# Performance work log

Hardware: AMD Instinct MI355X
Metric: run time of the kernel (lower is better)

## Reference

```python
import jax, jax.numpy as jnp
import numpy as np

EMBED_DIM = 2048
NUM_HEADS = 16
HEAD_DIM = EMBED_DIM // NUM_HEADS
EPS = 1e-6


def setup_inputs() -> dict:
    key = jax.random.key(0)
    ks = jax.random.split(key, 12)
    B, S, D = 4, 2048, EMBED_DIM
    s = 1.0 / np.sqrt(D)
    return {
        "query": jax.random.normal(ks[0], (B, S, D), jnp.float32),
        "key": jax.random.normal(ks[1], (B, S, D), jnp.float32),
        "value": jax.random.normal(ks[2], (B, S, D), jnp.float32),
        "Wq": jax.random.normal(ks[3], (D, D), jnp.float32) * s,
        "bq": jnp.zeros((D,), jnp.float32),
        "Wk": jax.random.normal(ks[4], (D, D), jnp.float32) * s,
        "bk": jnp.zeros((D,), jnp.float32),
        "Wv": jax.random.normal(ks[5], (D, D), jnp.float32) * s,
        "bv": jnp.zeros((D,), jnp.float32),
        "Wo": jax.random.normal(ks[6], (D, D), jnp.float32) * s,
        "bo": jnp.zeros((D,), jnp.float32),
        "q_norm_w": jnp.ones((HEAD_DIM,), jnp.float32),
        "k_norm_w": jnp.ones((HEAD_DIM,), jnp.float32),
    }


def _rms_norm(x, w):
    # RMSNorm over last dim (head_dim): x / sqrt(mean(x^2)+eps) * w
    ms = jnp.mean(jnp.square(x), axis=-1, keepdims=True)
    return x * jax.lax.rsqrt(ms + EPS) * w


def reference(query, key, value, Wq, bq, Wk, bk, Wv, bv, Wo, bo, q_norm_w, k_norm_w):
    B, Nq, D = query.shape
    Nk = key.shape[1]
    H, Hd = NUM_HEADS, HEAD_DIM
    # torch nn.Linear: y = x @ W.T + b
    q = (query @ Wq.T + bq).reshape(B, Nq, H, Hd).transpose(0, 2, 1, 3)  # (B,H,Nq,Hd)
    k = (key @ Wk.T + bk).reshape(B, Nk, H, Hd).transpose(0, 2, 1, 3)
    v = (value @ Wv.T + bv).reshape(B, Nk, H, Hd).transpose(0, 2, 1, 3)
    q = _rms_norm(q, q_norm_w)
    k = _rms_norm(k, k_norm_w)
    scale = 1.0 / np.sqrt(Hd)
    scores = jnp.einsum("bhqd,bhkd->bhqk", q, k) * scale  # (B,H,Nq,Nk)
    attn = jax.nn.softmax(scores, axis=-1)
    out = jnp.einsum("bhqk,bhkd->bhqd", attn, v)  # (B,H,Nq,Hd)
    out = out.transpose(0, 2, 1, 3).reshape(B, Nq, D)
    return out @ Wo.T + bo
```

## Files before the change

kernel.cpp:

```cpp
#include <hip/hip_runtime.h>

#define NB 4
#define NS 2048
#define ND 2048
#define NH 16
#define NHD 128

typedef __bf16 bf16;
typedef __attribute__((ext_vector_type(8))) __bf16 bf16x8;
typedef __attribute__((ext_vector_type(4))) __bf16 bf16x4;
typedef __attribute__((ext_vector_type(4))) float f32x4;
typedef __attribute__((ext_vector_type(16))) float f32x16;

#define MFMA(a, b, c) __builtin_amdgcn_mfma_f32_16x16x32_bf16(a, b, c, 0, 0, 0)
#define MFMA32(a, b, c) __builtin_amdgcn_mfma_f32_32x32x16_bf16(a, b, c, 0, 0, 0)

__device__ __forceinline__ void gload16(const bf16* g, bf16* l) {
    __builtin_amdgcn_global_load_lds(
        (const __attribute__((address_space(1))) void*)g,
        (__attribute__((address_space(3))) void*)l, 16, 0, 0);
}

#define BAR() do { asm volatile("" ::: "memory"); __builtin_amdgcn_s_barrier(); \
                   asm volatile("" ::: "memory"); } while (0)
#define VMCNT4() asm volatile("s_waitcnt vmcnt(4)" ::: "memory")
#define VMCNT0() asm volatile("s_waitcnt vmcnt(0)" ::: "memory")

enum { RA00 = 0, RA01 = 16384, RA10 = 32768, RA11 = 49152,
       RB00 = 65536, RB01 = 81920, RB10 = 98304, RB11 = 114688 };

__device__ __forceinline__ void stage_half(const bf16* gcorner, char* lds_region,
                                           int w, int lane, int scol) {
    const bf16* g = gcorner + (size_t)(w * 16 + (lane >> 3)) * ND + scol;
    gload16(g, (bf16*)(lds_region + w * 2048));
    gload16(g + (size_t)8 * ND, (bf16*)(lds_region + w * 2048 + 1024));
}

__device__ __forceinline__ void lds_loadA(const char* pool, int region, int mi0,
                                          int l15, int quad, bf16x8 (&af)[8]) {
    const int flip = (l15 & 4) << 3;
    #pragma unroll
    for (int mi = 0; mi < 4; ++mi) {
        const int rb = region + ((mi0 + mi) * 16 + l15) * 128;
        #pragma unroll
        for (int kk = 0; kk < 2; ++kk)
            af[mi * 2 + kk] = *reinterpret_cast<const bf16x8*>(
                pool + rb + ((kk * 64 + quad * 16) ^ flip));
    }
}

template <int NI0>
__device__ __forceinline__ void lds_loadB(const char* pool, int region, int wn1,
                                          int l15, int quad, bf16x8 (&bfr)[8]) {
    const int flip = (l15 & 4) << 3;
    #pragma unroll
    for (int ni = 0; ni < 2; ++ni) {
        const int rb = region + (wn1 * 64 + (NI0 + ni) * 16 + l15) * 128;
        #pragma unroll
        for (int kk = 0; kk < 2; ++kk)
            bfr[(NI0 + ni) * 2 + kk] = *reinterpret_cast<const bf16x8*>(
                pool + rb + ((kk * 64 + quad * 16) ^ flip));
    }
}

template <int MI0, int NI0>
__device__ __forceinline__ void mfma_quad(f32x4 (&acc)[8][4], const bf16x8 (&af)[8],
                                          const bf16x8 (&bfr)[8]) {
    __builtin_amdgcn_s_setprio(1);
    #pragma unroll
    for (int mi = 0; mi < 4; ++mi)
        #pragma unroll
        for (int ni = 0; ni < 2; ++ni)
            #pragma unroll
            for (int kk = 0; kk < 2; ++kk)
                acc[MI0 + mi][NI0 + ni] =
                    MFMA(af[mi * 2 + kk], bfr[(NI0 + ni) * 2 + kk], acc[MI0 + mi][NI0 + ni]);
    __builtin_amdgcn_s_setprio(0);
}

#define GEMM256_KLOOP(Ab, Bb)                                                        \
    stage_half(Ab, pool + RA00, w, lane, scol);                                      \
    stage_half(Ab + (size_t)128 * ND, pool + RA01, w, lane, scol);                   \
    stage_half(Bb, pool + RB00, w, lane, scol);                                      \
    stage_half(Bb + (size_t)128 * ND, pool + RB01, w, lane, scol);                   \
    stage_half(Bb + 64, pool + RB10, w, lane, scol);                                 \
    stage_half(Bb + (size_t)128 * ND + 64, pool + RB11, w, lane, scol);              \
    VMCNT4();                                                                        \
    BAR();                                                                           \
    for (int i = 0; i < 16; ++i) {                                                   \
        const int kA = (2 * i + 1) * 64;                                             \
        const int kN = (2 * i + 2) * 64;                                             \
        const int kN3 = (2 * i + 3) * 64;                                            \
                                                                             \
        lds_loadA(pool, rA0, 0, l15, quad, af);                                      \
        lds_loadB<0>(pool, rB0, wn1, l15, quad, bfr);                                \
        stage_half(Ab + kA, pool + RA10, w, lane, scol);                             \
        BAR(); mfma_quad<0, 0>(acc, af, bfr); BAR();                                 \
                                                                             \
        lds_loadB<2>(pool, rB0, wn1, l15, quad, bfr);                                \
        stage_half(Ab + (size_t)128 * ND + kA, pool + RA11, w, lane, scol);          \
        BAR(); mfma_quad<0, 2>(acc, af, bfr); BAR();                                 \
                                                                             \
        lds_loadA(pool, rA0, 4, l15, quad, af);                                      \
        stage_half(Bb + kN, pool + RB00, w, lane, scol);                             \
        BAR(); mfma_quad<4, 0>(acc, af, bfr); BAR();                                 \
                                                                             \
        stage_half(Bb + (size_t)128 * ND + kN, pool + RB01, w, lane, scol);          \
        VMCNT4();                                                                    \
        BAR(); mfma_quad<4, 2>(acc, af, bfr); BAR();                                 \
                                                                             \
        lds_loadA(pool, rA1, 0, l15, quad, af);                                      \
        lds_loadB<0>(pool, rB1, wn1, l15, quad, bfr);                                \
        stage_half(Ab + kN, pool + RA00, w, lane, scol);                             \
        BAR(); mfma_quad<0, 0>(acc, af, bfr); BAR();                                 \
                                                                             \
        lds_loadB<2>(pool, rB1, wn1, l15, quad, bfr);                                \
        stage_half(Ab + (size_t)128 * ND + kN, pool + RA01, w, lane, scol);          \
        BAR(); mfma_quad<0, 2>(acc, af, bfr); BAR();                                 \
                                                                             \
        lds_loadA(pool, rA1, 4, l15, quad, af);                                      \
        stage_half(Bb + kN3, pool + RB10, w, lane, scol);                            \
        BAR(); mfma_quad<4, 0>(acc, af, bfr); BAR();                                 \
                                                                             \
        stage_half(Bb + (size_t)128 * ND + kN3, pool + RB11, w, lane, scol);         \
        VMCNT4();                                                                    \
        BAR(); mfma_quad<4, 2>(acc, af, bfr); BAR();                                 \
    }

__global__ __launch_bounds__(256) void cvt_bf16(const float* __restrict__ src,
                                                bf16* __restrict__ dst)
{
    size_t i = ((size_t)blockIdx.x * 256 + threadIdx.x) * 8;
    float4 a = *reinterpret_cast<const float4*>(src + i);
    float4 b = *reinterpret_cast<const float4*>(src + i + 4);
    bf16x8 o;
    o[0] = (bf16)a.x; o[1] = (bf16)a.y; o[2] = (bf16)a.z; o[3] = (bf16)a.w;
    o[4] = (bf16)b.x; o[5] = (bf16)b.y; o[6] = (bf16)b.z; o[7] = (bf16)b.w;
    *reinterpret_cast<bf16x8*>(dst + i) = o;
}

__global__ __launch_bounds__(512, 2) void qkv_gemm(
    const bf16* __restrict__ Xb, const bf16* __restrict__ Wb,
    const float* __restrict__ bq, const float* __restrict__ bk, const float* __restrict__ bv,
    const float* __restrict__ qw, const float* __restrict__ kw,
    bf16* __restrict__ Oq, bf16* __restrict__ Ok, bf16* __restrict__ Ov)
{
    const int mat = blockIdx.z;
    const bf16* X     = Xb + (size_t)mat * (size_t)NB * NS * ND;
    const bf16* W     = Wb + (size_t)mat * ND * ND;
    const float* bias = (mat == 0) ? bq : (mat == 1) ? bk : bv;
    const float* nw   = (mat == 0) ? qw : kw;
    bf16* Out         = (mat == 0) ? Oq : (mat == 1) ? Ok : Ov;

    __shared__ alignas(1024) char pool[131072];
    __shared__ float red[256][4];
    __shared__ float scl[256][2];

    const int tid  = threadIdx.x;
    const int lane = tid & 63;
    const int w    = tid >> 6;
    const int wm   = w >> 2;
    const int wn   = w & 3;
    const int wn1  = wn & 1;
    const int quad = lane >> 4, l15 = lane & 15;

    const int m0 = blockIdx.y * 256;
    const int n0 = blockIdx.x * 256;

    const int scol = ((lane & 7) * 8) ^ ((lane & 32) ? 16 : 0);

    const int rA0 = RA00 + wm * 16384;
    const int rA1 = RA10 + wm * 16384;
    const int rB0 = RB00 + (wn >> 1) * 16384;
    const int rB1 = RB10 + (wn >> 1) * 16384;

    const bf16* Ab = X + (size_t)m0 * ND;
    const bf16* Bb = W + (size_t)n0 * ND;

    f32x4 acc[8][4] = {};
    bf16x8 af[8], bfr[8];

    GEMM256_KLOOP(Ab, Bb)

    #pragma unroll
    for (int ni = 0; ni < 4; ++ni) {
        float bn = bias[n0 + wn * 64 + ni * 16 + l15];
        #pragma unroll
        for (int mi = 0; mi < 8; ++mi)
            #pragma unroll
            for (int r = 0; r < 4; ++r)
                acc[mi][ni][r] += bn;
    }

    if (mat == 2) {
        bf16 (*Ts)[264] = (bf16(*)[264])pool;
        const int bb = m0 >> 11;
        const int s0 = m0 & (NS - 1);
        #pragma unroll
        for (int h2 = 0; h2 < 2; ++h2) {
            __syncthreads();
            if ((wn >> 1) == h2) {
                #pragma unroll
                for (int mi = 0; mi < 8; ++mi)
                    #pragma unroll
                    for (int ni = 0; ni < 4; ++ni) {
                        bf16x4 t;
                        #pragma unroll
                        for (int r = 0; r < 4; ++r) t[r] = (bf16)acc[mi][ni][r];
                        *reinterpret_cast<bf16x4*>(
                            &Ts[wn1 * 64 + ni * 16 + l15][wm * 128 + mi * 16 + quad * 4]) = t;
                    }
            }
            __syncthreads();
            const size_t obase = ((size_t)bb * NH + (n0 >> 7) + h2) * (size_t)NHD * NS;
            #pragma unroll
            for (int it = 0; it < 8; ++it) {
                int d = it * 16 + (tid >> 5);
                int c = (tid & 31) * 8;
                *reinterpret_cast<bf16x8*>(Out + obase + (size_t)d * NS + s0 + c) =
                    *reinterpret_cast<const bf16x8*>(&Ts[d][c]);
            }
        }
        return;
    }

    #pragma unroll
    for (int mi = 0; mi < 8; ++mi) {
        float ss[4];
        #pragma unroll
        for (int r = 0; r < 4; ++r) {
            float s = 0.f;
            #pragma unroll
            for (int ni = 0; ni < 4; ++ni) { float v = acc[mi][ni][r]; s += v * v; }
            ss[r] = s;
        }
        #pragma unroll
        for (int off = 1; off < 16; off <<= 1)
            #pragma unroll
            for (int r = 0; r < 4; ++r)
                ss[r] += __shfl_xor(ss[r], off);
        if (l15 == 0) {
            #pragma unroll
            for (int r = 0; r < 4; ++r)
                red[wm * 128 + mi * 16 + quad * 4 + r][wn] = ss[r];
        }
    }
    __syncthreads();
    {
        int row = tid >> 1, h2 = tid & 1;
        scl[row][h2] = rsqrtf((red[row][2 * h2] + red[row][2 * h2 + 1]) * (1.0f / 128.0f) + 1e-6f);
    }
    __syncthreads();

    const int hh = (n0 >> 7) + (wn >> 1);
    #pragma unroll
    for (int mi = 0; mi < 8; ++mi) {
        #pragma unroll
        for (int r = 0; r < 4; ++r) {
            int row = wm * 128 + mi * 16 + quad * 4 + r;
            int mg  = m0 + row;
            int bb  = mg >> 11;
            int ssi = mg & (NS - 1);
            size_t base = (((size_t)bb * NH + hh) * NS + ssi) * NHD;
            float sc_r = scl[row][wn >> 1];
            #pragma unroll
            for (int ni = 0; ni < 4; ++ni) {
                int col = (wn * 64 + ni * 16 + l15) & 127;
                Out[base + col] = (bf16)(acc[mi][ni][r] * sc_r * nw[col]);
            }
        }
    }
}

__global__ __launch_bounds__(512, 2) void flash_attn(
    const bf16* __restrict__ Q, const bf16* __restrict__ K, const bf16* __restrict__ Vt,
    bf16* __restrict__ O)
{
    __shared__ alignas(1024) char kpool[32768];
    __shared__ alignas(1024) char vpool[32768];
    __shared__ alignas(1024) char ppool[32768];

    const int tid  = threadIdx.x;
    const int lane = tid & 63;
    const int w    = tid >> 6;
    const int l31  = lane & 31;
    const int hi   = lane >> 5;
    const int b    = blockIdx.z, h = blockIdx.y;
    const int q0   = blockIdx.x * 256;
    const size_t hb = ((size_t)b * NH + h) * (size_t)NS * NHD;
    const bf16* Qh  = Q + hb;
    const bf16* Kh  = K + hb;
    const bf16* Vth = Vt + hb;

    bf16x8 qf[8];
    {
        const bf16* qrow = Qh + (size_t)(q0 + w * 32 + l31) * NHD + hi * 8;
        #pragma unroll
        for (int ks = 0; ks < 8; ++ks)
            qf[ks] = *reinterpret_cast<const bf16x8*>(qrow + ks * 16);
    }

    char* Psb = ppool + w * 4096;
    const int swz = (l31 & 7) << 4;
    const int qrow_b = l31 * 128;

    f32x16 o0 = {}, o1 = {}, o2 = {}, o3 = {};
    float m_r = -1e30f, l_r = 0.f;
    const float C = 0.12751740f;

    auto stage_tile = [&](int t, int bufsel) {
        const bf16* Kt  = Kh  + (size_t)(t & 31) * 64 * NHD;
        const bf16* Vtt = Vth + (size_t)(t & 31) * 64;
        char* Kb = kpool + bufsel * 16384;
        char* Vb = vpool + bufsel * 16384;
        #pragma unroll
        for (int j = 0; j < 2; ++j) {
            int c = w * 2 + j;
            int krow  = 4 * c + (lane >> 4);
            int kslot = (lane & 15) ^ (4 * (c & 1) + (lane >> 4));
            gload16(Kt + (size_t)krow * NHD + kslot * 8, (bf16*)(Kb + c * 1024));
            int vrow  = 8 * c + (lane >> 3);
            int vslot = (lane & 7) ^ (lane >> 3);
            gload16(Vtt + (size_t)vrow * NS + vslot * 8, (bf16*)(Vb + c * 1024));
        }
    };

    stage_tile(0, 0);

    const int NT = NS / 64;
    for (int kt = 0; kt < NT; ++kt) {
        const int cur = kt & 1;
        if (kt + 1 < NT) {
            stage_tile(kt + 1, cur ^ 1);
            VMCNT4();
        } else {
            VMCNT0();
        }
        BAR();

        const char* Kb = kpool + cur * 16384;
        const char* Vb = vpool + cur * 16384;

        f32x16 s0 = {}, s1 = {};
        __builtin_amdgcn_s_setprio(1);
        #pragma unroll
        for (int ks = 0; ks < 8; ++ks) {
            const int co = ks * 32 + hi * 16;
            bf16x8 k0 = *reinterpret_cast<const bf16x8*>(
                Kb + l31 * 256 + (co ^ swz));
            bf16x8 k1 = *reinterpret_cast<const bf16x8*>(
                Kb + (32 + l31) * 256 + (co ^ swz));
            s0 = MFMA32(k0, qf[ks], s0);
            s1 = MFMA32(k1, qf[ks], s1);
        }
        __builtin_amdgcn_s_setprio(0);

        float mt = s0[0];
        #pragma unroll
        for (int r = 1; r < 16; ++r) mt = fmaxf(mt, s0[r]);
        #pragma unroll
        for (int r = 0; r < 16; ++r) mt = fmaxf(mt, s1[r]);
        mt = fmaxf(mt, __shfl_xor(mt, 32));

        const bool grow = !__all(mt - m_r <= 64.0f);
        float alpha = 1.f;
        if (grow) {
            float mn = fmaxf(m_r, mt);
            alpha = __builtin_amdgcn_exp2f((m_r - mn) * C);
            m_r = mn;
        }
        const float mC = m_r * C;
        float rs = 0.f;
        #pragma unroll
        for (int r = 0; r < 16; ++r) { s0[r] = __builtin_amdgcn_exp2f(s0[r] * C - mC); rs += s0[r]; }
        #pragma unroll
        for (int r = 0; r < 16; ++r) { s1[r] = __builtin_amdgcn_exp2f(s1[r] * C - mC); rs += s1[r]; }
        rs += __shfl_xor(rs, 32);
        l_r = l_r * alpha + rs;

        #pragma unroll
        for (int g = 0; g < 4; ++g) {
            bf16x4 t0, t1;
            #pragma unroll
            for (int j = 0; j < 4; ++j) {
                t0[j] = (bf16)s0[g * 4 + j];
                t1[j] = (bf16)s1[g * 4 + j];
            }
            *reinterpret_cast<bf16x4*>(Psb + qrow_b + ((g * 16 + hi * 8) ^ swz)) = t0;
            *reinterpret_cast<bf16x4*>(Psb + qrow_b + ((64 + g * 16 + hi * 8) ^ swz)) = t1;
        }

        if (grow) {
            #pragma unroll
            for (int r = 0; r < 16; ++r) {
                float av = __shfl(alpha, (r & 3) + 8 * (r >> 2) + 4 * hi);
                o0[r] *= av; o1[r] *= av; o2[r] *= av; o3[r] *= av;
            }
        }

        __builtin_amdgcn_s_setprio(1);
        #pragma unroll
        for (int ks = 0; ks < 4; ++ks) {
            const int co = ks * 32 + hi * 16;
            bf16x8 pa = *reinterpret_cast<const bf16x8*>(Psb + qrow_b + (co ^ swz));
            bf16x8 v0 = *reinterpret_cast<const bf16x8*>(Vb + l31 * 128 + (co ^ swz));
            bf16x8 v1 = *reinterpret_cast<const bf16x8*>(Vb + (32 + l31) * 128 + (co ^ swz));
            bf16x8 v2 = *reinterpret_cast<const bf16x8*>(Vb + (64 + l31) * 128 + (co ^ swz));
            bf16x8 v3 = *reinterpret_cast<const bf16x8*>(Vb + (96 + l31) * 128 + (co ^ swz));
            o0 = MFMA32(pa, v0, o0);
            o1 = MFMA32(pa, v1, o1);
            o2 = MFMA32(pa, v2, o2);
            o3 = MFMA32(pa, v3, o3);
        }
        __builtin_amdgcn_s_setprio(0);

        BAR();
    }

    #pragma unroll
    for (int r = 0; r < 16; ++r) {
        int qp = (r & 3) + 8 * (r >> 2) + 4 * hi;
        float inv = 1.0f / __shfl(l_r, qp);
        int sg = q0 + w * 32 + qp;
        size_t base = ((size_t)b * NS + sg) * ND + (size_t)h * NHD + l31;
        O[base]      = (bf16)(o0[r] * inv);
        O[base + 32] = (bf16)(o1[r] * inv);
        O[base + 64] = (bf16)(o2[r] * inv);
        O[base + 96] = (bf16)(o3[r] * inv);
    }
}

__global__ __launch_bounds__(512, 2) void oproj_gemm(
    const bf16* __restrict__ A, const bf16* __restrict__ Wt,
    const float* __restrict__ bias, float* __restrict__ Out)
{
    __shared__ alignas(1024) char pool[131072];

    const int tid  = threadIdx.x;
    const int lane = tid & 63;
    const int w    = tid >> 6;
    const int wm   = w >> 2;
    const int wn   = w & 3;
    const int wn1  = wn & 1;
    const int quad = lane >> 4, l15 = lane & 15;

    const int m0 = blockIdx.y * 256;
    const int n0 = blockIdx.x * 256;

    const int scol = ((lane & 7) * 8) ^ ((lane & 32) ? 16 : 0);

    const int rA0 = RA00 + wm * 16384;
    const int rA1 = RA10 + wm * 16384;
    const int rB0 = RB00 + (wn >> 1) * 16384;
    const int rB1 = RB10 + (wn >> 1) * 16384;

    const bf16* Ab = A + (size_t)m0 * ND;
    const bf16* Bb = Wt + (size_t)n0 * ND;

    f32x4 acc[8][4] = {};
    bf16x8 af[8], bfr[8];

    GEMM256_KLOOP(Ab, Bb)

    #pragma unroll
    for (int ni = 0; ni < 4; ++ni) {
        int colg = n0 + wn * 64 + ni * 16 + l15;
        float bn = bias[colg];
        #pragma unroll
        for (int mi = 0; mi < 8; ++mi)
            #pragma unroll
            for (int r = 0; r < 4; ++r) {
                int mg = m0 + wm * 128 + mi * 16 + quad * 4 + r;
                Out[(size_t)mg * ND + colg] = acc[mi][ni][r] + bn;
            }
    }
}

extern "C" void kernel_launch(void* const* d_in, const int* in_sizes, int n_in,
                              void* d_out, int out_size, void* d_ws, size_t ws_size,
                              hipStream_t stream)
{
    const float* q  = (const float*)d_in[0];
    const float* k  = (const float*)d_in[1];
    const float* v  = (const float*)d_in[2];
    const float* Wq = (const float*)d_in[3];
    const float* bq = (const float*)d_in[4];
    const float* Wk = (const float*)d_in[5];
    const float* bk = (const float*)d_in[6];
    const float* Wv = (const float*)d_in[7];
    const float* bv = (const float*)d_in[8];
    const float* Wo = (const float*)d_in[9];
    const float* bo = (const float*)d_in[10];
    const float* qw = (const float*)d_in[11];
    const float* kw = (const float*)d_in[12];
    float* out = (float*)d_out;

    const size_t nX = (size_t)NB * NS * ND;
    const size_t nW = (size_t)ND * ND;

    bf16* Xb  = (bf16*)d_ws;
    bf16* Wb  = Xb + 3 * nX;
    bf16* Qn  = Wb + 4 * nW;
    bf16* Kn  = Qn + nX;
    bf16* Vtp = Kn + nX;
    bf16* Ob  = Xb;

    cvt_bf16<<<8192, 256, 0, stream>>>(q,  Xb);
    cvt_bf16<<<8192, 256, 0, stream>>>(k,  Xb + nX);
    cvt_bf16<<<8192, 256, 0, stream>>>(v,  Xb + 2 * nX);
    cvt_bf16<<<2048, 256, 0, stream>>>(Wq, Wb);
    cvt_bf16<<<2048, 256, 0, stream>>>(Wk, Wb + nW);
    cvt_bf16<<<2048, 256, 0, stream>>>(Wv, Wb + 2 * nW);
    cvt_bf16<<<2048, 256, 0, stream>>>(Wo, Wb + 3 * nW);

    qkv_gemm<<<dim3(8, 32, 3), dim3(512), 0, stream>>>(
        Xb, Wb, bq, bk, bv, qw, kw, Qn, Kn, Vtp);
    flash_attn<<<dim3(8, 16, 4), dim3(512), 0, stream>>>(Qn, Kn, Vtp, Ob);
    oproj_gemm<<<dim3(8, 32), dim3(512), 0, stream>>>(Ob, Wb + 3 * nW, bo, out);
}
```

Baseline: 739.2 us.

## Merge conversion launches and remap GEMM/attention blocks for XCD-aware L2 locality

Replaces seven separate fp32-to-bf16 conversion launches with one combined kernel that picks source and destination by block index, removing per-launch overhead and tail gaps. It also remaps the GEMM tile indices so that consecutive blocks dispatched round-robin across the eight XCDs share row panels on the same XCD. The attention grid is reordered so blocks of the same query tile, spread over all batch-heads, launch together. The aim is better L2 reuse per XCD at the cost of some index arithmetic.

```diff
diff --git a/kernel.cpp b/kernel.cpp
--- a/kernel.cpp
+++ b/kernel.cpp
@@ -127,16 +127,41 @@
         BAR(); mfma_quad<4, 2>(acc, af, bfr); BAR();                                 \
     }
 
-__global__ __launch_bounds__(256) void cvt_bf16(const float* __restrict__ src,
-                                                bf16* __restrict__ dst)
+__global__ __launch_bounds__(256) void cvt_all(
+    const float* __restrict__ q, const float* __restrict__ k, const float* __restrict__ v,
+    const float* __restrict__ Wq, const float* __restrict__ Wk,
+    const float* __restrict__ Wv, const float* __restrict__ Wo,
+    bf16* __restrict__ Xb, bf16* __restrict__ Wb)
 {
-    size_t i = ((size_t)blockIdx.x * 256 + threadIdx.x) * 8;
+    const size_t nX = (size_t)NB * NS * ND;
+    const size_t nW = (size_t)ND * ND;
+    int bid = blockIdx.x;
+    const float* src; bf16* dst;
+    if (bid < 24576) {
+        int sel = bid >> 13;
+        src = (sel == 0) ? q : (sel == 1) ? k : v;
+        dst = Xb + (size_t)sel * nX;
+        bid &= 8191;
+    } else {
+        int sel = (bid - 24576) >> 11;
+        src = (sel == 0) ? Wq : (sel == 1) ? Wk : (sel == 2) ? Wv : Wo;
+        dst = Wb + (size_t)sel * nW;
+        bid = (bid - 24576) & 2047;
+    }
+    size_t i = ((size_t)bid * 256 + threadIdx.x) * 8;
     float4 a = *reinterpret_cast<const float4*>(src + i);
     float4 b = *reinterpret_cast<const float4*>(src + i + 4);
     bf16x8 o;
     o[0] = (bf16)a.x; o[1] = (bf16)a.y; o[2] = (bf16)a.z; o[3] = (bf16)a.w;
     o[4] = (bf16)b.x; o[5] = (bf16)b.y; o[6] = (bf16)b.z; o[7] = (bf16)b.w;
     *reinterpret_cast<bf16x8*>(dst + i) = o;
+}
+
+__device__ __forceinline__ void gemm_remap(int flat, int& m0, int& n0) {
+    int xcd = flat & 7;
+    int idx = flat >> 3;
+    m0 = (xcd * 4 + (idx >> 3)) * 256;
+    n0 = (idx & 7) * 256;
 }
 
 __global__ __launch_bounds__(512, 2) void qkv_gemm(
@@ -164,8 +189,8 @@
     const int wn1  = wn & 1;
     const int quad = lane >> 4, l15 = lane & 15;
 
-    const int m0 = blockIdx.y * 256;
-    const int n0 = blockIdx.x * 256;
+    int m0, n0;
+    gemm_remap(blockIdx.y * 8 + blockIdx.x, m0, n0);
 
     const int scol = ((lane & 7) * 8) ^ ((lane & 32) ? 16 : 0);
 
@@ -285,8 +310,13 @@
     const int w    = tid >> 6;
     const int l31  = lane & 31;
     const int hi   = lane >> 5;
-    const int b    = blockIdx.z, h = blockIdx.y;
-    const int q0   = blockIdx.x * 256;
+
+    const int flat = (blockIdx.z * NH + blockIdx.y) * gridDim.x + blockIdx.x;
+    const int qt   = flat >> 6;
+    const int bh   = flat & 63;
+    const int b    = bh >> 4, h = bh & 15;
+    const int q0   = qt * 256;
+
     const size_t hb = ((size_t)b * NH + h) * (size_t)NS * NHD;
     const bf16* Qh  = Q + hb;
     const bf16* Kh  = K + hb;
@@ -444,8 +474,8 @@
     const int wn1  = wn & 1;
     const int quad = lane >> 4, l15 = lane & 15;
 
-    const int m0 = blockIdx.y * 256;
-    const int n0 = blockIdx.x * 256;
+    int m0, n0;
+    gemm_remap(blockIdx.y * 8 + blockIdx.x, m0, n0);
 
     const int scol = ((lane & 7) * 8) ^ ((lane & 32) ? 16 : 0);
 
@@ -505,13 +535,7 @@
     bf16* Vtp = Kn + nX;
     bf16* Ob  = Xb;
 
-    cvt_bf16<<<8192, 256, 0, stream>>>(q,  Xb);
-    cvt_bf16<<<8192, 256, 0, stream>>>(k,  Xb + nX);
-    cvt_bf16<<<8192, 256, 0, stream>>>(v,  Xb + 2 * nX);
-    cvt_bf16<<<2048, 256, 0, stream>>>(Wq, Wb);
-    cvt_bf16<<<2048, 256, 0, stream>>>(Wk, Wb + nW);
-    cvt_bf16<<<2048, 256, 0, stream>>>(Wv, Wb + 2 * nW);
-    cvt_bf16<<<2048, 256, 0, stream>>>(Wo, Wb + 3 * nW);
+    cvt_all<<<32768, 256, 0, stream>>>(q, k, v, Wq, Wk, Wv, Wo, Xb, Wb);
 
     qkv_gemm<<<dim3(8, 32, 3), dim3(512), 0, stream>>>(
         Xb, Wb, bq, bk, bv, qw, kw, Qn, Kn, Vtp);
```

New measurement: 714.9 us. 3.3% less time.
